# Kernel tuning notes

Measured on AMD Instinct MI355X. Metric: run time of the kernel, lower is better.

Reference implementation:

```python
import jax, jax.numpy as jnp
import numpy as np

EPS = 1e-5
B, F, C, H, L, S = 8192, 128, 256, 512, 4, 10


def _gelu(x):
    return jax.nn.gelu(x, approximate=False)  # torch nn.GELU default = exact erf


def _ln(x, g, b):
    m = jnp.mean(x, axis=-1, keepdims=True)
    v = jnp.var(x, axis=-1, keepdims=True)  # biased, matches torch LayerNorm
    return (x - m) / jnp.sqrt(v + EPS) * g + b


def setup_inputs() -> dict:
    key = jax.random.key(0)
    ks = iter(jax.random.split(key, 40))

    def w(shape, fan_in):
        return jax.random.normal(next(ks), shape, jnp.float32) / np.float32(np.sqrt(fan_in))

    def z0(*s):
        return jnp.zeros(s, jnp.float32)

    return dict(
        x=jax.random.normal(next(ks), (B, F), jnp.float32),
        context=jax.random.normal(next(ks), (B, C), jnp.float32),
        u=jax.random.normal(next(ks), (S, B, F), jnp.float32),
        Wi=w((F, H), F), bi=z0(H),
        Wt1=w((1, H), 1), bt1=z0(H), Wt2=w((H, H), H), bt2=z0(H),
        Wc1=w((C, 2 * H), C), bc1=z0(2 * H), Wc2=w((2 * H, H), 2 * H), bc2=z0(H),
        Wv=w((L, H, H), H), bv=z0(L, H), Woa=w((L, H, H), H), boa=z0(L, H),
        g1=jnp.ones((L, H), jnp.float32), be1=z0(L, H),
        Wm1=w((L, H, 4 * H), H), bm1=z0(L, 4 * H),
        Wm2=w((L, 4 * H, H), 4 * H), bm2=z0(L, H),
        g2=jnp.ones((L, H), jnp.float32), be2=z0(L, H),
        Wcv=w((L, H, H), H), bcv=z0(L, H), Wco=w((L, H, H), H), bco=z0(L, H),
        scale=0.5 * jnp.ones((L,), jnp.float32),
        Wp1=w((H, H), H), bp1=z0(H), Wp2=w((H, F), H), bp2=z0(F),
    )


def _forward(x, context, u, Wi, bi, Wt1, bt1, Wt2, bt2, Wc1, bc1, Wc2, bc2,
             Wv, bv, Woa, boa, g1, be1, Wm1, bm1, Wm2, bm2, g2, be2,
             Wcv, bcv, Wco, bco, scale, Wp1, bp1, Wp2, bp2):
    n_steps = u.shape[0]
    dt = 1.0 / n_steps
    nb = x.shape[0]
    nl = Wv.shape[0]

    # context projection, computed once as in torch
    ctx = _gelu(context @ Wc1 + bc1) @ Wc2 + bc2  # [B,H]
    # seq_len==1 cross-attention: softmax over a single key == 1, so the output
    # is out_proj(v_proj(ctx)) and does not depend on x -> precompute per layer.
    vctx = jnp.einsum('bh,lhk->lbk', ctx, Wcv) + bcv[:, None, :]    # [L,B,H]
    xatt = jnp.einsum('lbh,lhk->lbk', vctx, Wco) + bco[:, None, :]  # [L,B,H]

    def vel(z, t):
        tt = jnp.clip(t, 0.0, 1.0)[:, None]                          # [B,1]
        h = z @ Wi + bi + (_gelu(tt @ Wt1 + bt1) @ Wt2 + bt2)        # [B,H]
        for l in range(nl):
            # seq_len==1 self-attention collapses to out_proj(v_proj(h))
            attn = (h @ Wv[l] + bv[l]) @ Woa[l] + boa[l]
            h = _ln(h + attn, g1[l], be1[l])
            mlp = _gelu(h @ Wm1[l] + bm1[l]) @ Wm2[l] + bm2[l]
            h = _ln(h + mlp, g2[l], be2[l])
            h = h + scale[l] * xatt[l]
        return _gelu(h @ Wp1 + bp1) @ Wp2 + bp2                      # [B,F]

    def step(carry, inp):
        z, ld = carry
        t_val, u_k = inp
        t = jnp.full((nb,), t_val, jnp.float32)
        zs = jax.lax.stop_gradient(z)  # matches z.detach()/leaf z_req in torch
        v, Ju = jax.jvp(lambda zz: vel(zz, t), (zs,), (u_k,))
        ld = ld + jnp.sum(u_k * Ju, axis=-1) * dt  # Hutchinson u^T J u
        return (zs + v * dt, ld), None

    ts = jnp.arange(n_steps, dtype=jnp.float32) * dt
    (z, log_det), _ = jax.lax.scan(step, (x, jnp.zeros((nb,), jnp.float32)), (ts, u))
    return z, log_det


def reference(x, context, u, Wi, bi, Wt1, bt1, Wt2, bt2, Wc1, bc1, Wc2, bc2,
              Wv, bv, Woa, boa, g1, be1, Wm1, bm1, Wm2, bm2, g2, be2,
              Wcv, bcv, Wco, bco, scale, Wp1, bp1, Wp2, bp2):
    return _forward(x, context, u, Wi, bi, Wt1, bt1, Wt2, bt2, Wc1, bc1, Wc2, bc2,
                    Wv, bv, Woa, boa, g1, be1, Wm1, bm1, Wm2, bm2, g2, be2,
                    Wcv, bcv, Wco, bco, scale, Wp1, bp1, Wp2, bp2)
```

## Files before the change

kernel.cpp:

```cpp
#include <hip/hip_runtime.h>
#include <math.h>

using floatx4 = __attribute__((ext_vector_type(4))) float;
using bf16x8  = __attribute__((ext_vector_type(8))) __bf16;
using ushort8 = __attribute__((ext_vector_type(8))) unsigned short;

__device__ __forceinline__ float b2f(unsigned short u) {
  unsigned v = ((unsigned)u) << 16; float f; __builtin_memcpy(&f, &v, 4); return f;
}
__device__ __forceinline__ unsigned short f2b(float f) {
  unsigned u; __builtin_memcpy(&u, &f, 4);
  u += 0x7fffu + ((u >> 16) & 1u);
  return (unsigned short)(u >> 16);
}
__device__ __forceinline__ float gelu_f(float x) {
  return 0.5f * x * (1.0f + erff(x * 0.7071067811865475f));
}
__device__ __forceinline__ float gelu_d(float x) {
  float cdf = 0.5f * (1.0f + erff(x * 0.7071067811865475f));
  float pdf = 0.3989422804014327f * expf(-0.5f * x * x);
  return cdf + x * pdf;
}
__device__ __forceinline__ float wred(float v) {
  #pragma unroll
  for (int off = 32; off > 0; off >>= 1) v += __shfl_xor(v, off, 64);
  return v;
}
__device__ __forceinline__ void gload16(const unsigned short* g, unsigned short* l) {
  __builtin_amdgcn_global_load_lds(
      (__attribute__((address_space(1))) void*)(g),
      (__attribute__((address_space(3))) void*)(l), 16, 0, 0);
}

template<int MODE>
__global__ __launch_bounds__(256) void gemm_bt_k(
    const unsigned short* __restrict__ A, const unsigned short* __restrict__ Bt,
    void* __restrict__ C, const float* __restrict__ bias,
    const float* __restrict__ bias2, int M, int N, int K)
{
  __shared__ unsigned short As[128 * 32];
  __shared__ unsigned short Bs[128 * 32];
  const int tid  = threadIdx.x;
  const int lane = tid & 63;
  const int wave = tid >> 6;
  const int row0 = blockIdx.y * 128;
  const int col0 = blockIdx.x * 128;

  const int sr = wave * 32 + (lane >> 2);
  const int sk = (lane & 3) * 8;
  const unsigned short* Ag0 = A  + (size_t)(row0 + sr) * K + sk;
  const unsigned short* Ag1 = Ag0 + (size_t)16 * K;
  const unsigned short* Bg0 = Bt + (size_t)(col0 + sr) * K + sk;
  const unsigned short* Bg1 = Bg0 + (size_t)16 * K;
  unsigned short* As0 = &As[wave * 1024];
  unsigned short* Bs0 = &Bs[wave * 1024];

  const int wr = wave >> 1, wc = wave & 1;
  const int mrow = lane & 15;
  const int kq = (lane >> 4) * 8;

  floatx4 acc[4][4];
  const floatx4 zf4 = {0.f, 0.f, 0.f, 0.f};
  #pragma unroll
  for (int i = 0; i < 4; i++)
    #pragma unroll
    for (int j = 0; j < 4; j++) acc[i][j] = zf4;

  for (int k0 = 0; k0 < K; k0 += 32) {
    __syncthreads();
    gload16(Ag0 + k0, As0);
    gload16(Ag1 + k0, As0 + 512);
    gload16(Bg0 + k0, Bs0);
    gload16(Bg1 + k0, Bs0 + 512);
    __syncthreads();
    bf16x8 af[4], bfr[4];
    #pragma unroll
    for (int t = 0; t < 4; t++)
      af[t] = *(const bf16x8*)&As[(wr * 64 + t * 16 + mrow) * 32 + kq];
    #pragma unroll
    for (int t = 0; t < 4; t++)
      bfr[t] = *(const bf16x8*)&Bs[(wc * 64 + t * 16 + mrow) * 32 + kq];
    #pragma unroll
    for (int i = 0; i < 4; i++)
      #pragma unroll
      for (int j = 0; j < 4; j++)
        acc[i][j] = __builtin_amdgcn_mfma_f32_16x16x32_bf16(af[i], bfr[j], acc[i][j], 0, 0, 0);
  }

  const int quad = lane >> 4;
  const int cl = lane & 15;
  #pragma unroll
  for (int j = 0; j < 4; j++) {
    int col = col0 + wc * 64 + j * 16 + cl;
    float bb = bias ? bias[col] : 0.f;
    if (MODE >= 2) { if (bias2) bb += bias2[col]; }
    #pragma unroll
    for (int i = 0; i < 4; i++) {
      int rbase = row0 + wr * 64 + i * 16 + quad * 4;
      if (MODE == 3) {
        #pragma unroll
        for (int pp = 0; pp < 2; pp++) {
          float p = acc[i][j][2 * pp] + bb;
          float t = acc[i][j][2 * pp + 1];
          ((unsigned short*)C)[(size_t)(rbase + 2 * pp) * N + col]     = f2b(gelu_f(p));
          ((unsigned short*)C)[(size_t)(rbase + 2 * pp + 1) * N + col] = f2b(gelu_d(p) * t);
        }
      } else {
        #pragma unroll
        for (int rr = 0; rr < 4; rr++) {
          int row = rbase + rr;
          float v = acc[i][j][rr];
          if (MODE == 0 || MODE == 1) v += bb;
          if (MODE == 2 || MODE == 4) { if ((row & 1) == 0) v += bb; }
          if (MODE == 1) v = gelu_f(v);
          if (MODE == 4) ((float*)C)[(size_t)row * N + col] = v;
          else           ((unsigned short*)C)[(size_t)row * N + col] = f2b(v);
        }
      }
    }
  }
}

__global__ void transpose_cast_k(const float* __restrict__ W,
                                 unsigned short* __restrict__ Wt, int K, int N)
{
  __shared__ float tile[32][33];
  size_t off = (size_t)blockIdx.z * K * N;
  const float* Wp = W + off;
  unsigned short* Wtp = Wt + off;
  int bx = blockIdx.x, by = blockIdx.y;
  int tx = threadIdx.x, ty = threadIdx.y;
  #pragma unroll
  for (int i = ty; i < 32; i += 8)
    tile[i][tx] = Wp[(size_t)(by * 32 + i) * N + bx * 32 + tx];
  __syncthreads();
  #pragma unroll
  for (int i = ty; i < 32; i += 8)
    Wtp[(size_t)(bx * 32 + i) * K + by * 32 + tx] = f2b(tile[tx][i]);
}

__global__ __launch_bounds__(256) void combine_bias_k(
    const float* __restrict__ bvp, const float* __restrict__ Wb,
    const float* __restrict__ bo, float* __restrict__ bout, int H)
{
  int out = blockIdx.x * blockDim.x + threadIdx.x;
  int l   = blockIdx.y;
  const float* A2 = Wb + (size_t)l * H * H;
  float s = bo[(size_t)l * H + out];
  for (int k = 0; k < H; k++) s += bvp[(size_t)l * H + k] * A2[(size_t)k * H + out];
  bout[(size_t)l * H + out] = s;
}

__global__ __launch_bounds__(256) void ln_jvp_k(
    unsigned short* h, const unsigned short* __restrict__ r,
    const float* __restrict__ g, const float* __restrict__ be,
    const unsigned short* __restrict__ xatt, const float* __restrict__ sc_p,
    int Bhalf, int H)
{
  int gw = (int)((blockIdx.x * blockDim.x + threadIdx.x) >> 6);
  int lane = threadIdx.x & 63;
  if (gw >= Bhalf) return;
  int c0 = lane * 8;
  size_t op = (size_t)(2 * gw) * H + c0;
  size_t ot = op + H;
  ushort8 hp = *(const ushort8*)&h[op];
  ushort8 ht = *(const ushort8*)&h[ot];
  ushort8 rp = *(const ushort8*)&r[op];
  ushort8 rt = *(const ushort8*)&r[ot];
  float xv[8], dv[8];
  float s1 = 0.f, s2 = 0.f, sd = 0.f;
  #pragma unroll
  for (int j = 0; j < 8; j++) {
    xv[j] = b2f(hp[j]) + b2f(rp[j]);
    dv[j] = b2f(ht[j]) + b2f(rt[j]);
    s1 += xv[j]; s2 += xv[j] * xv[j]; sd += dv[j];
  }
  s1 = wred(s1); s2 = wred(s2); sd = wred(sd);
  float inv = 1.0f / (float)H;
  float m = s1 * inv;
  float var = s2 * inv - m * m;
  float rstd = rsqrtf(var + 1e-5f);
  float dm = sd * inv;
  float c = 0.f;
  #pragma unroll
  for (int j = 0; j < 8; j++) c += (xv[j] - m) * dv[j];
  c = wred(c);
  float cm = c * inv * rstd;
  float sl = sc_p ? *sc_p : 0.f;
  ushort8 oy, od;
  #pragma unroll
  for (int j = 0; j < 8; j++) {
    float xh = (xv[j] - m) * rstd;
    float gg = g[c0 + j];
    float y = xh * gg + be[c0 + j];
    if (xatt) y += sl * b2f(xatt[(size_t)gw * H + c0 + j]);
    float dy = gg * rstd * (dv[j] - dm - xh * cm);
    oy[j] = f2b(y); od[j] = f2b(dy);
  }
  *(ushort8*)&h[op] = oy;
  *(ushort8*)&h[ot] = od;
}

__global__ __launch_bounds__(256) void cast_k(const float* __restrict__ in,
                                              unsigned short* __restrict__ out, size_t n) {
  size_t i = blockIdx.x * blockDim.x + threadIdx.x;
  if (i < n) out[i] = f2b(in[i]);
}

__global__ __launch_bounds__(512) void temb_all_k(
    const float* __restrict__ Wt1, const float* __restrict__ bt1,
    const float* __restrict__ Wt2, const float* __restrict__ bt2,
    float dtv, float* __restrict__ tvecs, int H)
{
  __shared__ float e[512];
  int j = threadIdx.x;
  float t = fminf(fmaxf((float)blockIdx.x * dtv, 0.f), 1.f);
  e[j] = gelu_f(t * Wt1[j] + bt1[j]);
  __syncthreads();
  float s = bt2[j];
  for (int k = 0; k < H; k++) s += e[k] * Wt2[(size_t)k * H + j];
  tvecs[(size_t)blockIdx.x * H + j] = s;
}

__global__ __launch_bounds__(256) void init_k(
    const float* __restrict__ x, const float* __restrict__ u0,
    float* __restrict__ zf, float* __restrict__ ld,
    unsigned short* __restrict__ Abuf, int BF, int Bsz, int F)
{
  int i = (int)(blockIdx.x * blockDim.x + threadIdx.x);
  if (i < BF) {
    int r = i / F, c = i - r * F;
    float v = x[i];
    zf[i] = v;
    Abuf[(size_t)(2 * r) * F + c]     = f2b(v);
    Abuf[(size_t)(2 * r + 1) * F + c] = f2b(u0[i]);
  }
  if (i < Bsz) ld[i] = 0.f;
}

__global__ __launch_bounds__(256) void update_k(
    const float* __restrict__ vout, const float* __restrict__ u_next,
    const float* __restrict__ u_cur, float* __restrict__ zf,
    float* __restrict__ ld, unsigned short* __restrict__ Abuf,
    int Bsz, int F, float dtv)
{
  int wid = (int)((blockIdx.x * blockDim.x + threadIdx.x) >> 6);
  int lane = threadIdx.x & 63;
  if (wid >= Bsz) return;
  int c = lane * 2;
  size_t zo = (size_t)wid * F + c;
  size_t vp = (size_t)(2 * wid) * F + c;
  size_t vt = vp + F;
  float v0 = vout[vp], v1 = vout[vp + 1];
  float z0 = zf[zo] + v0 * dtv, z1 = zf[zo + 1] + v1 * dtv;
  zf[zo] = z0; zf[zo + 1] = z1;
  Abuf[vp] = f2b(z0); Abuf[vp + 1] = f2b(z1);
  float dot = u_cur[zo] * vout[vt] + u_cur[zo + 1] * vout[vt + 1];
  dot = wred(dot);
  if (lane == 0) ld[wid] += dot * dtv;
  if (u_next) { Abuf[vt] = f2b(u_next[zo]); Abuf[vt + 1] = f2b(u_next[zo + 1]); }
}

__global__ __launch_bounds__(256) void final_k(
    const float* __restrict__ zf, const float* __restrict__ ld,
    float* __restrict__ out, int BF, int Bsz)
{
  int i = (int)(blockIdx.x * blockDim.x + threadIdx.x);
  if (i < BF) out[i] = zf[i];
  if (i < Bsz) out[BF + i] = ld[i];
}

extern "C" void kernel_launch(void* const* d_in, const int* in_sizes, int n_in,
                              void* d_out, int out_size, void* d_ws, size_t ws_size,
                              hipStream_t stream) {
  constexpr int B = 8192, F = 128, C = 256, H = 512, L = 4, S = 10;
  constexpr int B2 = 2 * B;
  constexpr int BF = B * F;
  const float dtv = 1.0f / S;

  const float* x    = (const float*)d_in[0];
  const float* ctxI = (const float*)d_in[1];
  const float* u    = (const float*)d_in[2];
  const float* Wi   = (const float*)d_in[3];
  const float* bi   = (const float*)d_in[4];
  const float* Wt1  = (const float*)d_in[5];
  const float* bt1  = (const float*)d_in[6];
  const float* Wt2  = (const float*)d_in[7];
  const float* bt2  = (const float*)d_in[8];
  const float* Wc1  = (const float*)d_in[9];
  const float* bc1  = (const float*)d_in[10];
  const float* Wc2  = (const float*)d_in[11];
  const float* bc2  = (const float*)d_in[12];
  const float* Wv   = (const float*)d_in[13];
  const float* bv   = (const float*)d_in[14];
  const float* Woa  = (const float*)d_in[15];
  const float* boa  = (const float*)d_in[16];
  const float* g1   = (const float*)d_in[17];
  const float* be1  = (const float*)d_in[18];
  const float* Wm1  = (const float*)d_in[19];
  const float* bm1  = (const float*)d_in[20];
  const float* Wm2  = (const float*)d_in[21];
  const float* bm2  = (const float*)d_in[22];
  const float* g2   = (const float*)d_in[23];
  const float* be2  = (const float*)d_in[24];
  const float* Wcv  = (const float*)d_in[25];
  const float* bcv  = (const float*)d_in[26];
  const float* Wco  = (const float*)d_in[27];
  const float* bco  = (const float*)d_in[28];
  const float* scal = (const float*)d_in[29];
  const float* Wp1  = (const float*)d_in[30];
  const float* bp1  = (const float*)d_in[31];
  const float* Wp2  = (const float*)d_in[32];
  const float* bp2  = (const float*)d_in[33];

  char* wp = (char*)d_ws;
  auto alloc = [&](size_t bytes) -> void* {
    void* r = (void*)wp;
    wp += (bytes + 255) & ~(size_t)255;
    return r;
  };
  unsigned short* wWit  = (unsigned short*)alloc((size_t)H * F * 2);
  unsigned short* wWc1t = (unsigned short*)alloc((size_t)2 * H * C * 2);
  unsigned short* wWc2t = (unsigned short*)alloc((size_t)H * 2 * H * 2);
  unsigned short* wWvoT = (unsigned short*)alloc((size_t)L * H * H * 2);
  unsigned short* wCtxT = (unsigned short*)alloc((size_t)L * H * H * 2);
  unsigned short* wWm1t = (unsigned short*)alloc((size_t)L * 4 * H * H * 2);
  unsigned short* wWm2t = (unsigned short*)alloc((size_t)L * H * 4 * H * 2);
  unsigned short* wWp1t = (unsigned short*)alloc((size_t)H * H * 2);
  unsigned short* wWp2t = (unsigned short*)alloc((size_t)F * H * 2);
  unsigned short* wOaT  = (unsigned short*)alloc((size_t)L * H * H * 2);
  unsigned short* wCoT  = (unsigned short*)alloc((size_t)L * H * H * 2);
  unsigned short* wVb   = (unsigned short*)alloc((size_t)L * H * H * 2);
  unsigned short* wCvb  = (unsigned short*)alloc((size_t)L * H * H * 2);
  float* bvo            = (float*)alloc((size_t)L * H * 4);
  float* cbvo           = (float*)alloc((size_t)L * H * 4);
  float* tvecs          = (float*)alloc((size_t)S * H * 4);
  unsigned short* ctxc  = (unsigned short*)alloc((size_t)B * C * 2);
  unsigned short* Abuf  = (unsigned short*)alloc((size_t)B2 * F * 2);
  unsigned short* hbuf  = (unsigned short*)alloc((size_t)B2 * H * 2);
  unsigned short* tmp2  = (unsigned short*)alloc((size_t)B2 * H * 2);
  unsigned short* mbuf  = (unsigned short*)alloc((size_t)B2 * 4 * H * 2);
  unsigned short* xattb = (unsigned short*)alloc((size_t)L * B * H * 2);
  float* vout           = (float*)alloc((size_t)B2 * F * 4);
  float* zf             = (float*)alloc((size_t)B * F * 4);
  float* ldb            = (float*)alloc((size_t)B * 4);
  (void)ws_size; (void)in_sizes; (void)n_in; (void)out_size;

  auto T = [&](const float* W, unsigned short* Wt, int K, int N, int Lz) {
    dim3 g(N / 32, K / 32, Lz);
    transpose_cast_k<<<g, dim3(32, 8), 0, stream>>>(W, Wt, K, N);
  };
  auto G = [&](int mode, const unsigned short* A, const unsigned short* Bt, void* Cc,
               const float* bias, const float* bias2, int M, int N, int K) {
    dim3 g(N / 128, M / 128);
    switch (mode) {
      case 0: gemm_bt_k<0><<<g, 256, 0, stream>>>(A, Bt, Cc, bias, bias2, M, N, K); break;
      case 1: gemm_bt_k<1><<<g, 256, 0, stream>>>(A, Bt, Cc, bias, bias2, M, N, K); break;
      case 2: gemm_bt_k<2><<<g, 256, 0, stream>>>(A, Bt, Cc, bias, bias2, M, N, K); break;
      case 3: gemm_bt_k<3><<<g, 256, 0, stream>>>(A, Bt, Cc, bias, bias2, M, N, K); break;
      case 4: gemm_bt_k<4><<<g, 256, 0, stream>>>(A, Bt, Cc, bias, bias2, M, N, K); break;
    }
  };

  T(Wi,  wWit,  F, H, 1);
  T(Wc1, wWc1t, C, 2 * H, 1);
  T(Wc2, wWc2t, 2 * H, H, 1);
  T(Wm1, wWm1t, H, 4 * H, L);
  T(Wm2, wWm2t, 4 * H, H, L);
  T(Wp1, wWp1t, H, H, 1);
  T(Wp2, wWp2t, H, F, 1);
  T(Woa, wOaT, H, H, L);
  T(Wco, wCoT, H, H, L);
  cast_k<<<((size_t)L * H * H + 255) / 256, 256, 0, stream>>>(Wv,  wVb,  (size_t)L * H * H);
  cast_k<<<((size_t)L * H * H + 255) / 256, 256, 0, stream>>>(Wcv, wCvb, (size_t)L * H * H);
  for (int l = 0; l < L; l++) {
    size_t o2 = (size_t)l * H * H;
    G(0, wOaT + o2, wVb  + o2, wWvoT + o2, nullptr, nullptr, H, H, H);
    G(0, wCoT + o2, wCvb + o2, wCtxT + o2, nullptr, nullptr, H, H, H);
  }
  combine_bias_k<<<dim3(H / 256, L), 256, 0, stream>>>(bv,  Woa, boa, bvo,  H);
  combine_bias_k<<<dim3(H / 256, L), 256, 0, stream>>>(bcv, Wco, bco, cbvo, H);

  cast_k<<<(B * C + 255) / 256, 256, 0, stream>>>(ctxI, ctxc, (size_t)B * C);
  G(1, ctxc, wWc1t, mbuf, bc1, nullptr, B, 2 * H, C);
  G(0, mbuf, wWc2t, tmp2, bc2, nullptr, B, H, 2 * H);
  for (int l = 0; l < L; l++)
    G(0, tmp2, wCtxT + (size_t)l * H * H, xattb + (size_t)l * B * H,
      cbvo + l * H, nullptr, B, H, H);

  temb_all_k<<<S, H, 0, stream>>>(Wt1, bt1, Wt2, bt2, dtv, tvecs, H);
  init_k<<<(BF + 255) / 256, 256, 0, stream>>>(x, u, zf, ldb, Abuf, BF, B, F);

  for (int s = 0; s < S; s++) {
    G(2, Abuf, wWit, hbuf, bi, tvecs + (size_t)s * H, B2, H, F);
    for (int l = 0; l < L; l++) {
      size_t o2 = (size_t)l * H * H;
      size_t om = (size_t)l * 4 * H * H;
      G(2, hbuf, wWvoT + o2, tmp2, bvo + l * H, nullptr, B2, H, H);
      ln_jvp_k<<<B / 4, 256, 0, stream>>>(hbuf, tmp2, g1 + l * H, be1 + l * H,
                                          nullptr, nullptr, B, H);
      G(3, hbuf, wWm1t + om, mbuf, bm1 + (size_t)l * 4 * H, nullptr, B2, 4 * H, H);
      G(2, mbuf, wWm2t + om, tmp2, bm2 + l * H, nullptr, B2, H, 4 * H);
      ln_jvp_k<<<B / 4, 256, 0, stream>>>(hbuf, tmp2, g2 + l * H, be2 + l * H,
                                          xattb + (size_t)l * B * H, scal + l, B, H);
    }
    G(3, hbuf, wWp1t, tmp2, bp1, nullptr, B2, H, H);
    G(4, tmp2, wWp2t, vout, bp2, nullptr, B2, F, H);
    const float* u_cur = u + (size_t)s * BF;
    const float* u_next = (s + 1 < S) ? u + (size_t)(s + 1) * BF : nullptr;
    update_k<<<B / 4, 256, 0, stream>>>(vout, u_next, u_cur, zf, ldb, Abuf, B, F, dtv);
  }

  final_k<<<(BF + 255) / 256, 256, 0, stream>>>(zf, ldb, (float*)d_out, BF, B);
}
```

Baseline: 9.440 ms.

## Fuse residual LayerNorm-JVP into full-row GEMMs and fuse output GEMM with ODE update

Adds a GEMM kernel whose block owns 32 rows across all 512 output columns. The residual add, LayerNorm and its JVP tangent are computed in the epilogue, so the separate ln_jvp pass and the tmp2 round trip are gone. The final H->F projection is fused with the Euler update and the Hutchinson log-det accumulation, which removes the fp32 vout buffer and the update kernel. The cost is much larger LDS use, 32-row tiles that re-stream the full weight matrix per block with no double buffering, and fewer blocks for latency hiding.

```diff
diff --git a/kernel.cpp b/kernel.cpp
--- a/kernel.cpp
+++ b/kernel.cpp
@@ -20,11 +20,6 @@
   float cdf = 0.5f * (1.0f + erff(x * 0.7071067811865475f));
   float pdf = 0.3989422804014327f * expf(-0.5f * x * x);
   return cdf + x * pdf;
-}
-__device__ __forceinline__ float wred(float v) {
-  #pragma unroll
-  for (int off = 32; off > 0; off >>= 1) v += __shfl_xor(v, off, 64);
-  return v;
 }
 __device__ __forceinline__ void gload16(const unsigned short* g, unsigned short* l) {
   __builtin_amdgcn_global_load_lds(
@@ -111,14 +106,225 @@
           int row = rbase + rr;
           float v = acc[i][j][rr];
           if (MODE == 0 || MODE == 1) v += bb;
-          if (MODE == 2 || MODE == 4) { if ((row & 1) == 0) v += bb; }
+          if (MODE == 2) { if ((row & 1) == 0) v += bb; }
           if (MODE == 1) v = gelu_f(v);
-          if (MODE == 4) ((float*)C)[(size_t)row * N + col] = v;
-          else           ((unsigned short*)C)[(size_t)row * N + col] = f2b(v);
+          ((unsigned short*)C)[(size_t)row * N + col] = f2b(v);
         }
       }
     }
   }
+}
+
+template<bool XATT>
+__global__ __launch_bounds__(256) void gemm_ln_k(
+    const unsigned short* __restrict__ A, const unsigned short* __restrict__ Bt,
+    unsigned short* __restrict__ h, const float* __restrict__ bias,
+    const float* __restrict__ g, const float* __restrict__ be,
+    const unsigned short* __restrict__ xatt, const float* __restrict__ sc_p,
+    int K)
+{
+  constexpr int N = 512;
+  __shared__ unsigned short As[32 * 32];
+  __shared__ unsigned short Bs[512 * 32];
+  __shared__ unsigned short Hs[32 * 512];
+  __shared__ float red[16][4][4];
+  const int tid = threadIdx.x, lane = tid & 63, wave = tid >> 6;
+  const int row0 = blockIdx.x * 32;
+
+  #pragma unroll
+  for (int t = 0; t < 8; t++) {
+    int r = wave * 8 + t;
+    gload16(h + (size_t)(row0 + r) * N + lane * 8, &Hs[r * N]);
+  }
+
+  const int srb = lane >> 2;
+  const int sk  = (lane & 3) * 8;
+  const int mrow = lane & 15, kq = (lane >> 4) * 8;
+
+  floatx4 acc[2][8];
+  const floatx4 zf4 = {0.f, 0.f, 0.f, 0.f};
+  #pragma unroll
+  for (int i = 0; i < 2; i++)
+    #pragma unroll
+    for (int j = 0; j < 8; j++) acc[i][j] = zf4;
+
+  for (int k0 = 0; k0 < K; k0 += 32) {
+    __syncthreads();
+    if (wave < 2)
+      gload16(A + (size_t)(row0 + wave * 16 + srb) * K + k0 + sk, &As[wave * 512]);
+    #pragma unroll
+    for (int t = 0; t < 8; t++) {
+      int n = wave * 128 + t * 16;
+      gload16(Bt + (size_t)(n + srb) * K + k0 + sk, &Bs[n * 32]);
+    }
+    __syncthreads();
+    bf16x8 af[2], bfr[8];
+    #pragma unroll
+    for (int i = 0; i < 2; i++)
+      af[i] = *(const bf16x8*)&As[(i * 16 + mrow) * 32 + kq];
+    #pragma unroll
+    for (int j = 0; j < 8; j++)
+      bfr[j] = *(const bf16x8*)&Bs[(wave * 128 + j * 16 + mrow) * 32 + kq];
+    #pragma unroll
+    for (int i = 0; i < 2; i++)
+      #pragma unroll
+      for (int j = 0; j < 8; j++)
+        acc[i][j] = __builtin_amdgcn_mfma_f32_16x16x32_bf16(af[i], bfr[j], acc[i][j], 0, 0, 0);
+  }
+
+  const int quad = lane >> 4, cl = lane & 15;
+  float bc[8], gc[8], bec[8];
+  #pragma unroll
+  for (int j = 0; j < 8; j++) {
+    int col = wave * 128 + j * 16 + cl;
+    bc[j] = bias[col]; gc[j] = g[col]; bec[j] = be[col];
+  }
+
+  #pragma unroll
+  for (int i = 0; i < 2; i++) {
+    #pragma unroll
+    for (int rp = 0; rp < 2; rp++) {
+      int re = i * 16 + quad * 4 + rp * 2;
+      float sx = 0.f, sxx = 0.f, sdv = 0.f, sxdv = 0.f;
+      #pragma unroll
+      for (int j = 0; j < 8; j++) {
+        int col = wave * 128 + j * 16 + cl;
+        float xp = acc[i][j][rp * 2]     + bc[j] + b2f(Hs[re * N + col]);
+        float dv = acc[i][j][rp * 2 + 1]         + b2f(Hs[(re + 1) * N + col]);
+        sx += xp; sxx += xp * xp; sdv += dv; sxdv += xp * dv;
+      }
+      #pragma unroll
+      for (int off = 1; off <= 8; off <<= 1) {
+        sx   += __shfl_xor(sx, off, 64);
+        sxx  += __shfl_xor(sxx, off, 64);
+        sdv  += __shfl_xor(sdv, off, 64);
+        sxdv += __shfl_xor(sxdv, off, 64);
+      }
+      if (cl == 0) {
+        int pr = i * 8 + quad * 2 + rp;
+        red[pr][wave][0] = sx; red[pr][wave][1] = sxx;
+        red[pr][wave][2] = sdv; red[pr][wave][3] = sxdv;
+      }
+    }
+  }
+  __syncthreads();
+
+  const float inv = 1.0f / 512.0f;
+  float sl = 0.f;
+  if (XATT) sl = *sc_p;
+  #pragma unroll
+  for (int i = 0; i < 2; i++) {
+    #pragma unroll
+    for (int rp = 0; rp < 2; rp++) {
+      int pr = i * 8 + quad * 2 + rp;
+      float sx   = red[pr][0][0] + red[pr][1][0] + red[pr][2][0] + red[pr][3][0];
+      float sxx  = red[pr][0][1] + red[pr][1][1] + red[pr][2][1] + red[pr][3][1];
+      float sdv  = red[pr][0][2] + red[pr][1][2] + red[pr][2][2] + red[pr][3][2];
+      float sxdv = red[pr][0][3] + red[pr][1][3] + red[pr][2][3] + red[pr][3][3];
+      float m = sx * inv;
+      float var = sxx * inv - m * m;
+      float rstd = rsqrtf(var + 1e-5f);
+      float dm = sdv * inv;
+      float cm = (sxdv - m * sdv) * inv * rstd;
+      int re = i * 16 + quad * 4 + rp * 2;
+      size_t growe = (size_t)(row0 + re);
+      #pragma unroll
+      for (int j = 0; j < 8; j++) {
+        int col = wave * 128 + j * 16 + cl;
+        float xp = acc[i][j][rp * 2]     + bc[j] + b2f(Hs[re * N + col]);
+        float dv = acc[i][j][rp * 2 + 1]         + b2f(Hs[(re + 1) * N + col]);
+        float xh = (xp - m) * rstd;
+        float y = xh * gc[j] + bec[j];
+        if (XATT) y += sl * b2f(xatt[(growe >> 1) * N + col]);
+        float dy = gc[j] * rstd * (dv - dm - xh * cm);
+        h[growe * N + col]       = f2b(y);
+        h[(growe + 1) * N + col] = f2b(dy);
+      }
+    }
+  }
+}
+
+__global__ __launch_bounds__(256) void gemm_vout_k(
+    const unsigned short* __restrict__ A, const unsigned short* __restrict__ Bt,
+    const float* __restrict__ bias, const float* __restrict__ u_cur,
+    const float* __restrict__ u_next, float* __restrict__ zf,
+    float* __restrict__ ldb, unsigned short* __restrict__ Abuf,
+    int K, float dtv)
+{
+  constexpr int N = 128;
+  __shared__ unsigned short As[128 * 32];
+  __shared__ unsigned short Bs[128 * 32];
+  __shared__ float red[64][2];
+  const int tid = threadIdx.x, lane = tid & 63, wave = tid >> 6;
+  const int row0 = blockIdx.x * 128;
+
+  const int sr = wave * 32 + (lane >> 2);
+  const int sk = (lane & 3) * 8;
+  const unsigned short* Ag0 = A  + (size_t)(row0 + sr) * K + sk;
+  const unsigned short* Ag1 = Ag0 + (size_t)16 * K;
+  const unsigned short* Bg0 = Bt + (size_t)sr * K + sk;
+  const unsigned short* Bg1 = Bg0 + (size_t)16 * K;
+  unsigned short* As0 = &As[wave * 1024];
+  unsigned short* Bs0 = &Bs[wave * 1024];
+
+  const int wr = wave >> 1, wc = wave & 1;
+  const int mrow = lane & 15, kq = (lane >> 4) * 8;
+
+  floatx4 acc[4][4];
+  const floatx4 zf4 = {0.f, 0.f, 0.f, 0.f};
+  #pragma unroll
+  for (int i = 0; i < 4; i++)
+    #pragma unroll
+    for (int j = 0; j < 4; j++) acc[i][j] = zf4;
+
+  for (int k0 = 0; k0 < K; k0 += 32) {
+    __syncthreads();
+    gload16(Ag0 + k0, As0);
+    gload16(Ag1 + k0, As0 + 512);
+    gload16(Bg0 + k0, Bs0);
+    gload16(Bg1 + k0, Bs0 + 512);
+    __syncthreads();
+    bf16x8 af[4], bfr[4];
+    #pragma unroll
+    for (int t = 0; t < 4; t++)
+      af[t] = *(const bf16x8*)&As[(wr * 64 + t * 16 + mrow) * 32 + kq];
+    #pragma unroll
+    for (int t = 0; t < 4; t++)
+      bfr[t] = *(const bf16x8*)&Bs[(wc * 64 + t * 16 + mrow) * 32 + kq];
+    #pragma unroll
+    for (int i = 0; i < 4; i++)
+      #pragma unroll
+      for (int j = 0; j < 4; j++)
+        acc[i][j] = __builtin_amdgcn_mfma_f32_16x16x32_bf16(af[i], bfr[j], acc[i][j], 0, 0, 0);
+  }
+
+  const int quad = lane >> 4, cl = lane & 15;
+  #pragma unroll
+  for (int i = 0; i < 4; i++) {
+    #pragma unroll
+    for (int rp = 0; rp < 2; rp++) {
+      int rloc_e = wr * 64 + i * 16 + quad * 4 + rp * 2;
+      size_t growe = (size_t)(row0 + rloc_e);
+      size_t b = growe >> 1;
+      float dacc = 0.f;
+      #pragma unroll
+      for (int j = 0; j < 4; j++) {
+        int col = wc * 64 + j * 16 + cl;
+        float v  = acc[i][j][rp * 2] + bias[col];
+        float Ju = acc[i][j][rp * 2 + 1];
+        float z = zf[b * N + col] + v * dtv;
+        zf[b * N + col] = z;
+        Abuf[growe * N + col] = f2b(z);
+        if (u_next) Abuf[(growe + 1) * N + col] = f2b(u_next[b * N + col]);
+        dacc += u_cur[b * N + col] * Ju;
+      }
+      #pragma unroll
+      for (int off = 1; off <= 8; off <<= 1) dacc += __shfl_xor(dacc, off, 64);
+      if (cl == 0) red[wr * 32 + i * 8 + quad * 2 + rp][wc] = dacc;
+    }
+  }
+  __syncthreads();
+  if (tid < 64) ldb[(row0 >> 1) + tid] += (red[tid][0] + red[tid][1]) * dtv;
 }
 
 __global__ void transpose_cast_k(const float* __restrict__ W,
@@ -149,56 +355,6 @@
   float s = bo[(size_t)l * H + out];
   for (int k = 0; k < H; k++) s += bvp[(size_t)l * H + k] * A2[(size_t)k * H + out];
   bout[(size_t)l * H + out] = s;
-}
-
-__global__ __launch_bounds__(256) void ln_jvp_k(
-    unsigned short* h, const unsigned short* __restrict__ r,
-    const float* __restrict__ g, const float* __restrict__ be,
-    const unsigned short* __restrict__ xatt, const float* __restrict__ sc_p,
-    int Bhalf, int H)
-{
-  int gw = (int)((blockIdx.x * blockDim.x + threadIdx.x) >> 6);
-  int lane = threadIdx.x & 63;
-  if (gw >= Bhalf) return;
-  int c0 = lane * 8;
-  size_t op = (size_t)(2 * gw) * H + c0;
-  size_t ot = op + H;
-  ushort8 hp = *(const ushort8*)&h[op];
-  ushort8 ht = *(const ushort8*)&h[ot];
-  ushort8 rp = *(const ushort8*)&r[op];
-  ushort8 rt = *(const ushort8*)&r[ot];
-  float xv[8], dv[8];
-  float s1 = 0.f, s2 = 0.f, sd = 0.f;
-  #pragma unroll
-  for (int j = 0; j < 8; j++) {
-    xv[j] = b2f(hp[j]) + b2f(rp[j]);
-    dv[j] = b2f(ht[j]) + b2f(rt[j]);
-    s1 += xv[j]; s2 += xv[j] * xv[j]; sd += dv[j];
-  }
-  s1 = wred(s1); s2 = wred(s2); sd = wred(sd);
-  float inv = 1.0f / (float)H;
-  float m = s1 * inv;
-  float var = s2 * inv - m * m;
-  float rstd = rsqrtf(var + 1e-5f);
-  float dm = sd * inv;
-  float c = 0.f;
-  #pragma unroll
-  for (int j = 0; j < 8; j++) c += (xv[j] - m) * dv[j];
-  c = wred(c);
-  float cm = c * inv * rstd;
-  float sl = sc_p ? *sc_p : 0.f;
-  ushort8 oy, od;
-  #pragma unroll
-  for (int j = 0; j < 8; j++) {
-    float xh = (xv[j] - m) * rstd;
-    float gg = g[c0 + j];
-    float y = xh * gg + be[c0 + j];
-    if (xatt) y += sl * b2f(xatt[(size_t)gw * H + c0 + j]);
-    float dy = gg * rstd * (dv[j] - dm - xh * cm);
-    oy[j] = f2b(y); od[j] = f2b(dy);
-  }
-  *(ushort8*)&h[op] = oy;
-  *(ushort8*)&h[ot] = od;
 }
 
 __global__ __launch_bounds__(256) void cast_k(const float* __restrict__ in,
@@ -236,29 +392,6 @@
     Abuf[(size_t)(2 * r + 1) * F + c] = f2b(u0[i]);
   }
   if (i < Bsz) ld[i] = 0.f;
-}
-
-__global__ __launch_bounds__(256) void update_k(
-    const float* __restrict__ vout, const float* __restrict__ u_next,
-    const float* __restrict__ u_cur, float* __restrict__ zf,
-    float* __restrict__ ld, unsigned short* __restrict__ Abuf,
-    int Bsz, int F, float dtv)
-{
-  int wid = (int)((blockIdx.x * blockDim.x + threadIdx.x) >> 6);
-  int lane = threadIdx.x & 63;
-  if (wid >= Bsz) return;
-  int c = lane * 2;
-  size_t zo = (size_t)wid * F + c;
-  size_t vp = (size_t)(2 * wid) * F + c;
-  size_t vt = vp + F;
-  float v0 = vout[vp], v1 = vout[vp + 1];
-  float z0 = zf[zo] + v0 * dtv, z1 = zf[zo + 1] + v1 * dtv;
-  zf[zo] = z0; zf[zo + 1] = z1;
-  Abuf[vp] = f2b(z0); Abuf[vp + 1] = f2b(z1);
-  float dot = u_cur[zo] * vout[vt] + u_cur[zo + 1] * vout[vt + 1];
-  dot = wred(dot);
-  if (lane == 0) ld[wid] += dot * dtv;
-  if (u_next) { Abuf[vt] = f2b(u_next[zo]); Abuf[vt + 1] = f2b(u_next[zo + 1]); }
 }
 
 __global__ __launch_bounds__(256) void final_k(
@@ -341,7 +474,6 @@
   unsigned short* tmp2  = (unsigned short*)alloc((size_t)B2 * H * 2);
   unsigned short* mbuf  = (unsigned short*)alloc((size_t)B2 * 4 * H * 2);
   unsigned short* xattb = (unsigned short*)alloc((size_t)L * B * H * 2);
-  float* vout           = (float*)alloc((size_t)B2 * F * 4);
   float* zf             = (float*)alloc((size_t)B * F * 4);
   float* ldb            = (float*)alloc((size_t)B * 4);
   (void)ws_size; (void)in_sizes; (void)n_in; (void)out_size;
@@ -358,7 +490,6 @@
       case 1: gemm_bt_k<1><<<g, 256, 0, stream>>>(A, Bt, Cc, bias, bias2, M, N, K); break;
       case 2: gemm_bt_k<2><<<g, 256, 0, stream>>>(A, Bt, Cc, bias, bias2, M, N, K); break;
       case 3: gemm_bt_k<3><<<g, 256, 0, stream>>>(A, Bt, Cc, bias, bias2, M, N, K); break;
-      case 4: gemm_bt_k<4><<<g, 256, 0, stream>>>(A, Bt, Cc, bias, bias2, M, N, K); break;
     }
   };
 
@@ -396,19 +527,19 @@
     for (int l = 0; l < L; l++) {
       size_t o2 = (size_t)l * H * H;
       size_t om = (size_t)l * 4 * H * H;
-      G(2, hbuf, wWvoT + o2, tmp2, bvo + l * H, nullptr, B2, H, H);
-      ln_jvp_k<<<B / 4, 256, 0, stream>>>(hbuf, tmp2, g1 + l * H, be1 + l * H,
-                                          nullptr, nullptr, B, H);
+      gemm_ln_k<false><<<B2 / 32, 256, 0, stream>>>(
+          hbuf, wWvoT + o2, hbuf, bvo + l * H, g1 + l * H, be1 + l * H,
+          nullptr, nullptr, H);
       G(3, hbuf, wWm1t + om, mbuf, bm1 + (size_t)l * 4 * H, nullptr, B2, 4 * H, H);
-      G(2, mbuf, wWm2t + om, tmp2, bm2 + l * H, nullptr, B2, H, 4 * H);
-      ln_jvp_k<<<B / 4, 256, 0, stream>>>(hbuf, tmp2, g2 + l * H, be2 + l * H,
-                                          xattb + (size_t)l * B * H, scal + l, B, H);
+      gemm_ln_k<true><<<B2 / 32, 256, 0, stream>>>(
+          mbuf, wWm2t + om, hbuf, bm2 + l * H, g2 + l * H, be2 + l * H,
+          xattb + (size_t)l * B * H, scal + l, 4 * H);
     }
     G(3, hbuf, wWp1t, tmp2, bp1, nullptr, B2, H, H);
-    G(4, tmp2, wWp2t, vout, bp2, nullptr, B2, F, H);
     const float* u_cur = u + (size_t)s * BF;
     const float* u_next = (s + 1 < S) ? u + (size_t)(s + 1) * BF : nullptr;
-    update_k<<<B / 4, 256, 0, stream>>>(vout, u_next, u_cur, zf, ldb, Abuf, B, F, dtv);
+    gemm_vout_k<<<B2 / 128, 256, 0, stream>>>(
+        tmp2, wWp2t, bp2, u_cur, u_next, zf, ldb, Abuf, H, dtv);
   }
 
   final_k<<<(BF + 255) / 256, 256, 0, stream>>>(zf, ldb, (float*)d_out, BF, B);
```

After: 9.553 ms. No clear change (+1.2%).
